# Optimization experiments

Hardware: AMD Instinct MI355X
Metric: run time of the kernel (lower is better)

The kernel has to match this reference:

```python
import jax, jax.numpy as jnp
import numpy as np

N_NODES = 100000


def sage_conv(x, src, dst, W_l, b_l, W_r):
    # PyG SAGEConv (aggr='mean'): out = lin_l(mean_{j->i} x_j) + lin_r(x_i)
    # lin_l has bias, lin_r does not.
    msgs = x[src]                                             # [E, d_in] irregular gather
    summed = jax.ops.segment_sum(msgs, dst, num_segments=N_NODES)
    deg = jax.ops.segment_sum(jnp.ones((src.shape[0],), x.dtype), dst,
                              num_segments=N_NODES)
    mean = summed / jnp.maximum(deg, 1.0)[:, None]            # [N, d_in]
    return mean @ W_l.T + b_l + x @ W_r.T                     # [N, d_out]


def setup_inputs() -> dict:
    key = jax.random.key(0)
    ks = jax.random.split(key, 8)
    input_dim, hidden_dim, output_dim = 64, 128, 64
    E = 1600000
    x = jax.random.normal(ks[0], (N_NODES, input_dim), dtype=jnp.float32)
    edge_index = jax.random.randint(ks[1], (2, E), 0, N_NODES, dtype=jnp.int64)

    def glorot(k, shape):
        lim = (6.0 / (shape[0] + shape[1])) ** 0.5
        return jax.random.uniform(k, shape, jnp.float32, -lim, lim)

    W1_l = glorot(ks[2], (hidden_dim, input_dim))
    b1 = jnp.zeros((hidden_dim,), jnp.float32)
    W1_r = glorot(ks[3], (hidden_dim, input_dim))
    W2_l = glorot(ks[4], (output_dim, hidden_dim))
    b2 = jnp.zeros((output_dim,), jnp.float32)
    W2_r = glorot(ks[5], (output_dim, hidden_dim))
    return {"x": x, "edge_index": edge_index,
            "W1_l": W1_l, "b1": b1, "W1_r": W1_r,
            "W2_l": W2_l, "b2": b2, "W2_r": W2_r}


def reference(x, edge_index, W1_l, b1, W1_r, W2_l, b2, W2_r):
    src, dst = edge_index[0], edge_index[1]
    h = jax.nn.relu(sage_conv(x, src, dst, W1_l, b1, W1_r))
    h = jax.nn.relu(sage_conv(h, src, dst, W2_l, b2, W2_r))
    # Original module computes norm(x) and dropout(x) but discards the results,
    # so the returned value is just the second ReLU output.
    return h
```

## Files before the change

kernel.cpp:

```cpp
#include <hip/hip_runtime.h>
#include <hip/hip_bf16.h>


#define NODE_DIM0 64
#define NPBK 512
#define MAXB 256
#define CAPB 12288
#define EPB  4096

__device__ inline unsigned short f2bf(float f) {
    unsigned u = __float_as_uint(f);
    return (unsigned short)((u + 0x7fffu + ((u >> 16) & 1u)) >> 16);
}


__global__ __launch_bounds__(256) void bucket_scatter(const int* __restrict__ src,
                                                      const int* __restrict__ dst,
                                                      int* __restrict__ gcur,
                                                      unsigned* __restrict__ pairs, int E) {
    __shared__ int hist[MAXB];
    __shared__ int incl[MAXB];
    __shared__ int exoff[MAXB];
    __shared__ int cur[MAXB];
    __shared__ int chunkBase[MAXB];
    __shared__ unsigned staged[EPB];
    __shared__ unsigned char sbkt[EPB];
    const int t = threadIdx.x;
    const int base = blockIdx.x * EPB;
    int cnt = E - base; if (cnt > EPB) cnt = EPB;

    hist[t] = 0;
    __syncthreads();

    int myS[16], myD[16];
#pragma unroll
    for (int it = 0; it < 16; ++it) {
        int e = base + it * 256 + t;
        if (e < E) {
            myS[it] = src[e];
            myD[it] = dst[e];
            atomicAdd(&hist[myD[it] >> 9], 1);
        } else {
            myD[it] = -1;
        }
    }
    __syncthreads();

    incl[t] = hist[t];
    __syncthreads();
    for (int o = 1; o < 256; o <<= 1) {
        int add = (t >= o) ? incl[t - o] : 0;
        __syncthreads();
        incl[t] += add;
        __syncthreads();
    }
    exoff[t] = incl[t] - hist[t];
    cur[t] = 0;
    chunkBase[t] = (hist[t] > 0) ? atomicAdd(&gcur[t], hist[t]) : 0;
    __syncthreads();

#pragma unroll
    for (int it = 0; it < 16; ++it) {
        if (myD[it] >= 0) {
            int b = myD[it] >> 9;
            int p = exoff[b] + atomicAdd(&cur[b], 1);
            staged[p] = ((unsigned)(myD[it] & (NPBK - 1)) << 17) | (unsigned)myS[it];
            sbkt[p] = (unsigned char)b;
        }
    }
    __syncthreads();

    for (int p = t; p < cnt; p += 256) {
        int b = sbkt[p];
        int g = chunkBase[b] + (p - exoff[b]);
        if (g < CAPB) pairs[(size_t)b * CAPB + g] = staged[p];
    }
}


__global__ __launch_bounds__(256) void bucket_csr(const unsigned* __restrict__ pairs,
                                                  const int* __restrict__ gcur,
                                                  int* __restrict__ startA,
                                                  int* __restrict__ degA,
                                                  int* __restrict__ esrc, int N) {
    __shared__ int ldeg[NPBK];
    __shared__ int scn[NPBK];
    __shared__ int lcur[NPBK];
    __shared__ int lsrc[CAPB];
    const int b = blockIdx.x;
    const int t = threadIdx.x;
    const int node0 = b * NPBK;
    int cnt = gcur[b]; if (cnt > CAPB) cnt = CAPB;

    ldeg[t] = 0; ldeg[t + 256] = 0;
    __syncthreads();

    const unsigned* reg = pairs + (size_t)b * CAPB;
    for (int i = t; i < cnt; i += 256)
        atomicAdd(&ldeg[reg[i] >> 17], 1);
    __syncthreads();

    scn[t] = ldeg[t]; scn[t + 256] = ldeg[t + 256];
    __syncthreads();
    for (int o = 1; o < NPBK; o <<= 1) {
        int a0 = (t >= o) ? scn[t - o] : 0;
        int a1 = (t + 256 >= o) ? scn[t + 256 - o] : 0;
        __syncthreads();
        scn[t] += a0; scn[t + 256] += a1;
        __syncthreads();
    }
    int e0 = scn[t] - ldeg[t];
    int e1 = scn[t + 256] - ldeg[t + 256];
    lcur[t] = e0; lcur[t + 256] = e1;
    const int gbase = b * CAPB;
    if (node0 + t < N)       { startA[node0 + t] = gbase + e0;       degA[node0 + t] = ldeg[t]; }
    if (node0 + 256 + t < N) { startA[node0 + 256 + t] = gbase + e1; degA[node0 + 256 + t] = ldeg[t + 256]; }
    __syncthreads();

    for (int i = t; i < cnt; i += 256) {
        unsigned w = reg[i];
        int pos = atomicAdd(&lcur[w >> 17], 1);
        lsrc[pos] = (int)(w & 0x1FFFFu);
    }
    __syncthreads();

    int* out = esrc + (size_t)b * CAPB;
    for (int i = t; i < cnt; i += 256) out[i] = lsrc[i];
}


__global__ void cast_bf(const float* __restrict__ in, unsigned short* __restrict__ out, int n4) {
    int i = blockIdx.x * 256 + threadIdx.x;
    if (i < n4) {
        float4 v = ((const float4*)in)[i];
        ushort4 o;
        o.x = f2bf(v.x); o.y = f2bf(v.y); o.z = f2bf(v.z); o.w = f2bf(v.w);
        ((ushort4*)out)[i] = o;
    }
}

__global__ void cast_weights(const float* __restrict__ a, const float* __restrict__ b,
                             const float* __restrict__ c, const float* __restrict__ d,
                             unsigned short* __restrict__ oa, unsigned short* __restrict__ ob,
                             unsigned short* __restrict__ oc, unsigned short* __restrict__ od) {
    int i = blockIdx.x * 256 + threadIdx.x;
    if (i < 8192) {
        oa[i] = f2bf(a[i]); ob[i] = f2bf(b[i]);
        oc[i] = f2bf(c[i]); od[i] = f2bf(d[i]);
    }
}


template <int MODE>
__global__ __launch_bounds__(256) void gather64(const unsigned short* __restrict__ feat,
                                                const int* __restrict__ startA,
                                                const int* __restrict__ degA,
                                                const int* __restrict__ esrc,
                                                const unsigned short* __restrict__ sdata,
                                                unsigned short* __restrict__ meanOut,
                                                float* __restrict__ outF, int n) {
    const int w = (blockIdx.x * 256 + threadIdx.x) >> 3;
    const int fl = threadIdx.x & 7;
    if (w >= n) return;
    const int s0 = startA[w], dg = degA[w];
    float acc[8] = {0.f, 0.f, 0.f, 0.f, 0.f, 0.f, 0.f, 0.f};
    const int* ep = esrc + s0;
    int e = 0;
    for (; e + 8 <= dg; e += 8) {
        int s_[8];
#pragma unroll
        for (int k = 0; k < 8; ++k) s_[k] = ep[e + k];
        uint4 u[8];
#pragma unroll
        for (int k = 0; k < 8; ++k)
            u[k] = *(const uint4*)(feat + (size_t)s_[k] * 64 + fl * 8);
#pragma unroll
        for (int k = 0; k < 8; ++k) {
            acc[0] += __uint_as_float(u[k].x << 16);
            acc[1] += __uint_as_float(u[k].x & 0xffff0000u);
            acc[2] += __uint_as_float(u[k].y << 16);
            acc[3] += __uint_as_float(u[k].y & 0xffff0000u);
            acc[4] += __uint_as_float(u[k].z << 16);
            acc[5] += __uint_as_float(u[k].z & 0xffff0000u);
            acc[6] += __uint_as_float(u[k].w << 16);
            acc[7] += __uint_as_float(u[k].w & 0xffff0000u);
        }
    }
    for (; e < dg; ++e) {
        uint4 u = *(const uint4*)(feat + (size_t)ep[e] * 64 + fl * 8);
        acc[0] += __uint_as_float(u.x << 16);
        acc[1] += __uint_as_float(u.x & 0xffff0000u);
        acc[2] += __uint_as_float(u.y << 16);
        acc[3] += __uint_as_float(u.y & 0xffff0000u);
        acc[4] += __uint_as_float(u.z << 16);
        acc[5] += __uint_as_float(u.z & 0xffff0000u);
        acc[6] += __uint_as_float(u.w << 16);
        acc[7] += __uint_as_float(u.w & 0xffff0000u);
    }
    const float inv = 1.0f / fmaxf((float)dg, 1.0f);
    if (MODE == 0) {
        unsigned us[8];
#pragma unroll
        for (int q = 0; q < 8; ++q) us[q] = f2bf(acc[q] * inv);
        uint4 o4;
        o4.x = us[0] | (us[1] << 16);
        o4.y = us[2] | (us[3] << 16);
        o4.z = us[4] | (us[5] << 16);
        o4.w = us[6] | (us[7] << 16);
        *(uint4*)(meanOut + (size_t)w * 64 + fl * 8) = o4;
    } else {
        uint4 us = *(const uint4*)(sdata + (size_t)w * 64 + fl * 8);
        float sv8[8];
        sv8[0] = __uint_as_float(us.x << 16);
        sv8[1] = __uint_as_float(us.x & 0xffff0000u);
        sv8[2] = __uint_as_float(us.y << 16);
        sv8[3] = __uint_as_float(us.y & 0xffff0000u);
        sv8[4] = __uint_as_float(us.z << 16);
        sv8[5] = __uint_as_float(us.z & 0xffff0000u);
        sv8[6] = __uint_as_float(us.w << 16);
        sv8[7] = __uint_as_float(us.w & 0xffff0000u);
        float4 o0, o1;
        o0.x = fmaxf(acc[0] * inv + sv8[0], 0.f);
        o0.y = fmaxf(acc[1] * inv + sv8[1], 0.f);
        o0.z = fmaxf(acc[2] * inv + sv8[2], 0.f);
        o0.w = fmaxf(acc[3] * inv + sv8[3], 0.f);
        o1.x = fmaxf(acc[4] * inv + sv8[4], 0.f);
        o1.y = fmaxf(acc[5] * inv + sv8[5], 0.f);
        o1.z = fmaxf(acc[6] * inv + sv8[6], 0.f);
        o1.w = fmaxf(acc[7] * inv + sv8[7], 0.f);
        *(float4*)(outF + (size_t)w * 64 + fl * 8)     = o0;
        *(float4*)(outF + (size_t)w * 64 + fl * 8 + 4) = o1;
    }
}


__global__ __launch_bounds__(256) void fused_l12(const unsigned short* __restrict__ meanb,
                                                 const unsigned short* __restrict__ selfb,
                                                 const unsigned short* __restrict__ W1l,
                                                 const float* __restrict__ b1,
                                                 const unsigned short* __restrict__ W1r,
                                                 const unsigned short* __restrict__ W2l,
                                                 const float* __restrict__ b2,
                                                 const unsigned short* __restrict__ W2r,
                                                 unsigned short* __restrict__ zout,
                                                 unsigned short* __restrict__ sout, int n) {
    using bf16x8 = __attribute__((ext_vector_type(8))) short;
    using f32x4  = __attribute__((ext_vector_type(4))) float;
    constexpr int LDW = 136;
    __shared__ unsigned short h1t[16 * LDW];
    const int wv   = threadIdx.x >> 6;
    const int lane = threadIdx.x & 63;
    const int row16 = lane & 15;
    const int quad  = lane >> 4;

    bf16x8 bl1[2][2], br1[2][2];
    float bv1[2];
#pragma unroll
    for (int r = 0; r < 2; ++r) {
        int nc = (wv * 2 + r) * 16 + row16;
#pragma unroll
        for (int kk = 0; kk < 2; ++kk) {
            bl1[r][kk] = *(const bf16x8*)(W1l + (size_t)nc * 64 + kk * 32 + quad * 8);
            br1[r][kk] = *(const bf16x8*)(W1r + (size_t)nc * 64 + kk * 32 + quad * 8);
        }
        bv1[r] = b1[nc];
    }
    const int nc2 = wv * 16 + row16;
    bf16x8 bl2[4], br2[4];
#pragma unroll
    for (int kk = 0; kk < 4; ++kk) {
        bl2[kk] = *(const bf16x8*)(W2l + (size_t)nc2 * 128 + kk * 32 + quad * 8);
        br2[kk] = *(const bf16x8*)(W2r + (size_t)nc2 * 128 + kk * 32 + quad * 8);
    }
    const float bv2 = b2[nc2];

    const int mtiles = n / 16;
    for (int mt = blockIdx.x; mt < mtiles; mt += gridDim.x) {
        const int m = mt * 16 + row16;
        bf16x8 am[2], as2[2];
#pragma unroll
        for (int kk = 0; kk < 2; ++kk) {
            am[kk]  = *(const bf16x8*)(meanb + (size_t)m * 64 + kk * 32 + quad * 8);
            as2[kk] = *(const bf16x8*)(selfb + (size_t)m * 64 + kk * 32 + quad * 8);
        }
#pragma unroll
        for (int r = 0; r < 2; ++r) {
            f32x4 acc = {0.f, 0.f, 0.f, 0.f};
#pragma unroll
            for (int kk = 0; kk < 2; ++kk)
                acc = __builtin_amdgcn_mfma_f32_16x16x32_bf16(am[kk], bl1[r][kk], acc, 0, 0, 0);
#pragma unroll
            for (int kk = 0; kk < 2; ++kk)
                acc = __builtin_amdgcn_mfma_f32_16x16x32_bf16(as2[kk], br1[r][kk], acc, 0, 0, 0);
            const int nc = (wv * 2 + r) * 16 + row16;
#pragma unroll
            for (int i = 0; i < 4; ++i)
                h1t[(quad * 4 + i) * LDW + nc] = f2bf(fmaxf(acc[i] + bv1[r], 0.f));
        }
        __syncthreads();
        bf16x8 a2[4];
#pragma unroll
        for (int kk = 0; kk < 4; ++kk)
            a2[kk] = *(const bf16x8*)(h1t + row16 * LDW + kk * 32 + quad * 8);
        f32x4 accz = {0.f, 0.f, 0.f, 0.f};
        f32x4 accs = {0.f, 0.f, 0.f, 0.f};
#pragma unroll
        for (int kk = 0; kk < 4; ++kk) {
            accz = __builtin_amdgcn_mfma_f32_16x16x32_bf16(a2[kk], bl2[kk], accz, 0, 0, 0);
            accs = __builtin_amdgcn_mfma_f32_16x16x32_bf16(a2[kk], br2[kk], accs, 0, 0, 0);
        }
        const int rowb = mt * 16 + quad * 4;
#pragma unroll
        for (int i = 0; i < 4; ++i) {
            zout[(size_t)(rowb + i) * 64 + nc2] = f2bf(accz[i]);
            sout[(size_t)(rowb + i) * 64 + nc2] = f2bf(accs[i] + bv2);
        }
        __syncthreads();
    }
}


static inline char* align_up(char* p, size_t a) {
    return (char*)(((uintptr_t)p + a - 1) & ~(uintptr_t)(a - 1));
}

extern "C" void kernel_launch(void* const* d_in, const int* in_sizes, int n_in,
                              void* d_out, int out_size, void* d_ws, size_t ws_size,
                              hipStream_t stream) {
    const float* x   = (const float*)d_in[0];
    const int*   ei  = (const int*)d_in[1];
    const float* W1l = (const float*)d_in[2];
    const float* b1  = (const float*)d_in[3];
    const float* W1r = (const float*)d_in[4];
    const float* W2l = (const float*)d_in[5];
    const float* b2  = (const float*)d_in[6];
    const float* W2r = (const float*)d_in[7];
    float* out = (float*)d_out;

    const int N = in_sizes[0] / NODE_DIM0;
    const int E = in_sizes[1] / 2;
    const int* src = ei;
    const int* dst = ei + E;
    const int nbuck = (N + NPBK - 1) / NPBK;

    char* p = (char*)d_ws;
    int* gcur   = (int*)p; p += (size_t)MAXB * 4;          p = align_up(p, 16);
    int* startA = (int*)p; p += (size_t)N * 4;             p = align_up(p, 16);
    int* degA   = (int*)p; p += (size_t)N * 4;             p = align_up(p, 16);
    int* esrc   = (int*)p; p += (size_t)nbuck * CAPB * 4;  p = align_up(p, 16);
    unsigned short* xbf   = (unsigned short*)p; p += (size_t)N * 64 * 2;
    unsigned short* scr2  = (unsigned short*)p; p += (size_t)N * 128 * 2;
    unsigned short* wl1bf = (unsigned short*)p; p += (size_t)128 * 64 * 2;
    unsigned short* wr1bf = (unsigned short*)p; p += (size_t)128 * 64 * 2;
    unsigned short* wl2bf = (unsigned short*)p; p += (size_t)64 * 128 * 2;
    unsigned short* wr2bf = (unsigned short*)p; p += (size_t)64 * 128 * 2;
    unsigned short* meanbf = (unsigned short*)p; p += (size_t)N * 64 * 2;

    unsigned* pairs = (unsigned*)scr2;
    unsigned short* zbf = scr2;
    unsigned short* sbf = scr2 + (size_t)N * 64;

    hipMemsetAsync(gcur, 0, (size_t)MAXB * 4, stream);
    bucket_scatter<<<(E + EPB - 1) / EPB, 256, 0, stream>>>(src, dst, gcur, pairs, E);
    bucket_csr<<<nbuck, 256, 0, stream>>>(pairs, gcur, startA, degA, esrc, N);

    cast_bf<<<(N * 64 / 4 + 255) / 256, 256, 0, stream>>>(x, xbf, N * 64 / 4);
    cast_weights<<<32, 256, 0, stream>>>(W1l, W1r, W2l, W2r, wl1bf, wr1bf, wl2bf, wr2bf);

    gather64<0><<<(N * 8 + 255) / 256, 256, 0, stream>>>(xbf, startA, degA, esrc, nullptr, meanbf, nullptr, N);

    fused_l12<<<1024, 256, 0, stream>>>(meanbf, xbf, wl1bf, b1, wr1bf,
                                        wl2bf, b2, wr2bf, zbf, sbf, N);

    gather64<1><<<(N * 8 + 255) / 256, 256, 0, stream>>>(zbf, startA, degA, esrc, sbf, nullptr, out, N);
}
```

Baseline: 228.1 us.

## Halve CSR bucket size and sort each node's edges by source slice

Buckets now cover 256 nodes instead of 512, giving 512 buckets with smaller per-bucket capacity. Within each bucket, edges are counting-sorted by node and then by a coarse source-index slice (src>>13), so each node's neighbor list is ordered by source region. This should improve cache locality of the later feature gathers and lower per-block shared memory use. The cost is a larger scan (16 counters per node) and a smaller bucket capacity (5120), which risks overflow and silently dropped edges on skewed degree distributions.

```diff
diff --git a/kernel.cpp b/kernel.cpp
--- a/kernel.cpp
+++ b/kernel.cpp
@@ -3,10 +3,11 @@
 
 
 #define NODE_DIM0 64
-#define NPBK 512
-#define MAXB 256
-#define CAPB 12288
+#define NPBK 256
+#define MAXB 512
+#define CAPB 5120
 #define EPB  4096
+#define NSL  16
 
 __device__ inline unsigned short f2bf(float f) {
     unsigned u = __float_as_uint(f);
@@ -24,12 +25,12 @@
     __shared__ int cur[MAXB];
     __shared__ int chunkBase[MAXB];
     __shared__ unsigned staged[EPB];
-    __shared__ unsigned char sbkt[EPB];
+    __shared__ unsigned short sbkt[EPB];
     const int t = threadIdx.x;
     const int base = blockIdx.x * EPB;
     int cnt = E - base; if (cnt > EPB) cnt = EPB;
 
-    hist[t] = 0;
+    hist[t] = 0; hist[t + 256] = 0;
     __syncthreads();
 
     int myS[16], myD[16];
@@ -39,33 +40,36 @@
         if (e < E) {
             myS[it] = src[e];
             myD[it] = dst[e];
-            atomicAdd(&hist[myD[it] >> 9], 1);
+            atomicAdd(&hist[myD[it] >> 8], 1);
         } else {
             myD[it] = -1;
         }
     }
     __syncthreads();
 
-    incl[t] = hist[t];
-    __syncthreads();
-    for (int o = 1; o < 256; o <<= 1) {
-        int add = (t >= o) ? incl[t - o] : 0;
-        __syncthreads();
-        incl[t] += add;
+    incl[t] = hist[t]; incl[t + 256] = hist[t + 256];
+    __syncthreads();
+    for (int o = 1; o < MAXB; o <<= 1) {
+        int a0 = (t >= o) ? incl[t - o] : 0;
+        int a1 = (t + 256 >= o) ? incl[t + 256 - o] : 0;
+        __syncthreads();
+        incl[t] += a0; incl[t + 256] += a1;
         __syncthreads();
     }
     exoff[t] = incl[t] - hist[t];
-    cur[t] = 0;
+    exoff[t + 256] = incl[t + 256] - hist[t + 256];
+    cur[t] = 0; cur[t + 256] = 0;
     chunkBase[t] = (hist[t] > 0) ? atomicAdd(&gcur[t], hist[t]) : 0;
+    chunkBase[t + 256] = (hist[t + 256] > 0) ? atomicAdd(&gcur[t + 256], hist[t + 256]) : 0;
     __syncthreads();
 
 #pragma unroll
     for (int it = 0; it < 16; ++it) {
         if (myD[it] >= 0) {
-            int b = myD[it] >> 9;
+            int b = myD[it] >> 8;
             int p = exoff[b] + atomicAdd(&cur[b], 1);
             staged[p] = ((unsigned)(myD[it] & (NPBK - 1)) << 17) | (unsigned)myS[it];
-            sbkt[p] = (unsigned char)b;
+            sbkt[p] = (unsigned short)b;
         }
     }
     __syncthreads();
@@ -83,43 +87,47 @@
                                                   int* __restrict__ startA,
                                                   int* __restrict__ degA,
                                                   int* __restrict__ esrc, int N) {
-    __shared__ int ldeg[NPBK];
-    __shared__ int scn[NPBK];
-    __shared__ int lcur[NPBK];
+    __shared__ int ldeg[NPBK * NSL];
+    __shared__ int lcur[NPBK * NSL];
     __shared__ int lsrc[CAPB];
+    __shared__ int wsum[256];
     const int b = blockIdx.x;
     const int t = threadIdx.x;
-    const int node0 = b * NPBK;
     int cnt = gcur[b]; if (cnt > CAPB) cnt = CAPB;
 
-    ldeg[t] = 0; ldeg[t + 256] = 0;
+    for (int i = t; i < NPBK * NSL; i += 256) ldeg[i] = 0;
     __syncthreads();
 
     const unsigned* reg = pairs + (size_t)b * CAPB;
-    for (int i = t; i < cnt; i += 256)
-        atomicAdd(&ldeg[reg[i] >> 17], 1);
-    __syncthreads();
-
-    scn[t] = ldeg[t]; scn[t + 256] = ldeg[t + 256];
-    __syncthreads();
-    for (int o = 1; o < NPBK; o <<= 1) {
-        int a0 = (t >= o) ? scn[t - o] : 0;
-        int a1 = (t + 256 >= o) ? scn[t + 256 - o] : 0;
-        __syncthreads();
-        scn[t] += a0; scn[t + 256] += a1;
-        __syncthreads();
-    }
-    int e0 = scn[t] - ldeg[t];
-    int e1 = scn[t + 256] - ldeg[t + 256];
-    lcur[t] = e0; lcur[t + 256] = e1;
-    const int gbase = b * CAPB;
-    if (node0 + t < N)       { startA[node0 + t] = gbase + e0;       degA[node0 + t] = ldeg[t]; }
-    if (node0 + 256 + t < N) { startA[node0 + 256 + t] = gbase + e1; degA[node0 + 256 + t] = ldeg[t + 256]; }
-    __syncthreads();
-
     for (int i = t; i < cnt; i += 256) {
         unsigned w = reg[i];
-        int pos = atomicAdd(&lcur[w >> 17], 1);
+        atomicAdd(&ldeg[((w >> 17) << 4) | ((w & 0x1FFFFu) >> 13)], 1);
+    }
+    __syncthreads();
+
+    const int base = t * NSL;
+    int run = 0, loc[NSL];
+#pragma unroll
+    for (int k = 0; k < NSL; ++k) { loc[k] = run; run += ldeg[base + k]; }
+    wsum[t] = run;
+    __syncthreads();
+    for (int o = 1; o < 256; o <<= 1) {
+        int add = (t >= o) ? wsum[t - o] : 0;
+        __syncthreads();
+        wsum[t] += add;
+        __syncthreads();
+    }
+    const int excl = wsum[t] - run;
+#pragma unroll
+    for (int k = 0; k < NSL; ++k) lcur[base + k] = excl + loc[k];
+    const int node0 = b * NPBK;
+    if (node0 + t < N) { startA[node0 + t] = b * CAPB + excl; degA[node0 + t] = run; }
+    __syncthreads();
+
+    for (int i = t; i < cnt; i += 256) {
+        unsigned w = reg[i];
+        int key = ((w >> 17) << 4) | ((w & 0x1FFFFu) >> 13);
+        int pos = atomicAdd(&lcur[key], 1);
         lsrc[pos] = (int)(w & 0x1FFFFu);
     }
     __syncthreads();
```

After: 224.5 us. About the same (-1.6%).
